# Kernel optimization log

Hardware: AMD Instinct MI355X
Metric: run time of the kernel (lower is better)

The kernel has to match this reference:

```python
import jax, jax.numpy as jnp
import numpy as np

HEADS = 16
LN_EPS = 1e-5


def setup_inputs() -> dict:
    key = jax.random.key(0)
    ks = jax.random.split(key, 4)
    B, S, C, U = 2, 2048, 1024, 1024
    scale = 1.0 / np.sqrt(C)
    return {
        "inputs": jax.random.normal(ks[0], (B, S, C), dtype=jnp.float32),
        "Wq": jax.random.normal(ks[1], (C, U), dtype=jnp.float32) * scale,
        "bq": jnp.zeros((U,), dtype=jnp.float32),
        "Wk": jax.random.normal(ks[2], (C, U), dtype=jnp.float32) * scale,
        "bk": jnp.zeros((U,), dtype=jnp.float32),
        "Wv": jax.random.normal(ks[3], (C, U), dtype=jnp.float32) * scale,
        "bv": jnp.zeros((U,), dtype=jnp.float32),
        "ln_gamma": jnp.ones((S, U), dtype=jnp.float32),
        "ln_beta": jnp.zeros((S, U), dtype=jnp.float32),
    }


def reference(inputs, Wq, bq, Wk, bk, Wv, bv, ln_gamma, ln_beta):
    B, S, C = inputs.shape
    U = Wq.shape[1]
    H = HEADS
    dh = U // H

    Q = inputs @ Wq + bq  # [B,S,U]
    K = inputs @ Wk + bk
    V = inputs @ Wv + bv

    # torch: concat(split(X, U//H, dim=-1), dim=0) -> head-major stacking on batch
    def split_heads(X):
        return jnp.moveaxis(X.reshape(B, S, H, dh), 2, 0).reshape(H * B, S, dh)

    Q_, K_, V_ = split_heads(Q), split_heads(K), split_heads(V)

    scores = jnp.einsum('bqd,bkd->bqk', Q_, K_) / jnp.sqrt(jnp.float32(dh))
    tri = jnp.tril(jnp.ones((S, S), dtype=bool))  # causal mask
    scores = jnp.where(tri[None, :, :], scores, jnp.float32(-1e9))
    attn = jax.nn.softmax(scores, axis=-1)
    out_ = jnp.einsum('bqk,bkd->bqd', attn, V_)  # [H*B,S,dh]

    # inverse: split on batch into H chunks of size B, concat on feature dim
    out = jnp.moveaxis(out_.reshape(H, B, S, dh), 0, 2).reshape(B, S, U)

    out = out + inputs  # residual

    # LayerNorm over normalized_shape=[S, U] (joint seq+feature stats)
    mu = jnp.mean(out, axis=(-2, -1), keepdims=True)
    var = jnp.mean(jnp.square(out - mu), axis=(-2, -1), keepdims=True)
    out = (out - mu) / jnp.sqrt(var + LN_EPS) * ln_gamma + ln_beta
    return out
```

## Files before the change

kernel.cpp:

```cpp
#include <hip/hip_runtime.h>
#include <hip/hip_bf16.h>


typedef __bf16 bf16_t;
typedef __bf16 bf16x8 __attribute__((ext_vector_type(8)));
typedef __bf16 bf16x4 __attribute__((ext_vector_type(4)));
typedef _Float16 f16_t;
typedef _Float16 f16x2 __attribute__((ext_vector_type(2)));
typedef _Float16 f16x4 __attribute__((ext_vector_type(4)));
typedef _Float16 f16x8 __attribute__((ext_vector_type(8)));
typedef float f32x4 __attribute__((ext_vector_type(4)));

constexpr int Bsz = 2;
constexpr int Seq = 2048;
constexpr int Cdim = 1024;
constexpr int Udim = 1024;
constexpr int Hn = 16;
constexpr int Dh = 64;
constexpr int Mrows = Bsz * Seq;
constexpr int PerBatch = Seq * Udim;
constexpr float SCLQ = 0.125f * 1.44269504088896340736f;

__device__ __forceinline__ void gload16(const void* g, void* l)
{
    __builtin_amdgcn_global_load_lds(
        (const __attribute__((address_space(1))) void*)g,
        (__attribute__((address_space(3))) void*)l, 16, 0, 0);
}

__device__ __forceinline__ f16x2 pkrtz(float a, float b)
{
    return __builtin_bit_cast(f16x2, __builtin_amdgcn_cvt_pkrtz(a, b));
}

__global__ __launch_bounds__(256)
void prep(const float* __restrict__ X,
          const float* __restrict__ Wq, const float* __restrict__ Wk,
          const float* __restrict__ Wv,
          bf16_t* __restrict__ Xb,
          bf16_t* __restrict__ Tq, bf16_t* __restrict__ Tk,
          bf16_t* __restrict__ Tv, float* __restrict__ stats)
{
    int z = blockIdx.z;
    int tid = threadIdx.x;
    if (z < 3) {
        const float* W = (z == 0) ? Wq : (z == 1) ? Wk : Wv;
        bf16_t* T = (z == 0) ? Tq : (z == 1) ? Tk : Tv;
        __shared__ bf16_t t[64][65];
        int x0 = blockIdx.x * 64, y0 = blockIdx.y * 64;
        int tx = tid & 63, ty = tid >> 6;
        for (int i = ty; i < 64; i += 4)
            t[i][tx] = (bf16_t)W[(size_t)(y0 + i) * Cdim + x0 + tx];
        __syncthreads();
        for (int i = ty; i < 64; i += 4)
            T[(size_t)(x0 + i) * Cdim + y0 + tx] = t[tx][i];
    } else {
        int bi = blockIdx.y * 16 + blockIdx.x;
        if (bi == 0 && tid < 4) stats[tid] = 0.0f;
        const float4* Xv = (const float4*)X;
#pragma unroll
        for (int k = 0; k < 16; k++) {
            int i = bi * 4096 + k * 256 + tid;
            float4 v = Xv[i];
            bf16x4 o = { (bf16_t)v.x, (bf16_t)v.y, (bf16_t)v.z, (bf16_t)v.w };
            *(bf16x4*)(Xb + (size_t)i * 4) = o;
        }
    }
}

__global__ __launch_bounds__(256)
void gemm_qkv(const bf16_t* __restrict__ X,
              const bf16_t* __restrict__ Wt0, const bf16_t* __restrict__ Wt1,
              const bf16_t* __restrict__ Wt2,
              const float* __restrict__ b0, const float* __restrict__ b1,
              const float* __restrict__ b2,
              f16_t* __restrict__ O0, f16_t* __restrict__ O1, f16_t* __restrict__ O2v)
{
    int z = blockIdx.z;
    const bf16_t* Wt = (z == 0) ? Wt0 : (z == 1) ? Wt1 : Wt2;
    const float* bias = (z == 0) ? b0 : (z == 1) ? b1 : b2;
    float scl = (z == 0) ? SCLQ : 1.0f;

    constexpr int Kd = 1024, Nd = 1024;
    __shared__ __align__(16) bf16_t As[128 * 32];
    __shared__ __align__(16) bf16_t Bs[128 * 32];

    int tid = threadIdx.x;
    int wave = tid >> 6, lane = tid & 63, quad = lane >> 4, l16 = lane & 15;
    int wm = (wave & 1) * 64, wn = (wave >> 1) * 64;
    int m0 = blockIdx.y * 128, n0 = blockIdx.x * 128;

    f32x4 acc[4][4] = {};

    int e0 = wave * 512 + lane * 8;
    int r0 = e0 >> 5, c0 = e0 & 31;
    int e1 = e0 + 2048;
    int r1 = e1 >> 5, c1 = e1 & 31;
    const bf16_t* Ag = X + (size_t)m0 * Kd;
    const bf16_t* Bg = Wt + (size_t)n0 * Kd;
    bf16_t* AsW0 = As + wave * 512;
    bf16_t* AsW1 = As + 2048 + wave * 512;
    bf16_t* BsW0 = Bs + wave * 512;
    bf16_t* BsW1 = Bs + 2048 + wave * 512;

    for (int k0 = 0; k0 < Kd; k0 += 32) {
        gload16(Ag + (size_t)r0 * Kd + k0 + c0, AsW0);
        gload16(Ag + (size_t)r1 * Kd + k0 + c1, AsW1);
        gload16(Bg + (size_t)r0 * Kd + k0 + c0, BsW0);
        gload16(Bg + (size_t)r1 * Kd + k0 + c1, BsW1);
        __syncthreads();

        bf16x8 af[4], bfr[4];
#pragma unroll
        for (int i = 0; i < 4; i++)
            af[i] = *(const bf16x8*)&As[(wm + i * 16 + l16) * 32 + quad * 8];
#pragma unroll
        for (int i = 0; i < 4; i++)
            bfr[i] = *(const bf16x8*)&Bs[(wn + i * 16 + l16) * 32 + quad * 8];
#pragma unroll
        for (int mt = 0; mt < 4; mt++)
#pragma unroll
            for (int nt = 0; nt < 4; nt++)
                acc[mt][nt] = __builtin_amdgcn_mfma_f32_16x16x32_bf16(
                    af[mt], bfr[nt], acc[mt][nt], 0, 0, 0);
        __syncthreads();
    }

    if (z < 2) {
        f16_t* Og = (z == 0) ? O0 : O1;
#pragma unroll
        for (int nt = 0; nt < 4; nt++) {
            int col = n0 + wn + nt * 16 + l16;
            float bv = bias[col];
#pragma unroll
            for (int mt = 0; mt < 4; mt++) {
                int row = m0 + wm + mt * 16 + quad * 4;
#pragma unroll
                for (int r = 0; r < 4; r++)
                    Og[(size_t)(row + r) * Nd + col] = (f16_t)((acc[mt][nt][r] + bv) * scl);
            }
        }
    } else {
        int bb = m0 >> 11;
#pragma unroll
        for (int nt = 0; nt < 4; nt++) {
            int col = n0 + wn + nt * 16 + l16;
            float bv = bias[col];
            int h = col >> 6, d = col & 63;
            f16_t* vbase = O2v + (((size_t)(bb * Hn + h) * Dh + d) << 11);
#pragma unroll
            for (int mt = 0; mt < 4; mt++) {
                int row = m0 + wm + mt * 16 + quad * 4;
                int s = row & (Seq - 1);
                f16x4 pk;
#pragma unroll
                for (int r = 0; r < 4; r++) pk[r] = (f16_t)(acc[mt][nt][r] + bv);
                *(f16x4*)(vbase + s) = pk;
            }
        }
    }
}

__global__ __launch_bounds__(256)
void attn7(const f16_t* __restrict__ Q, const f16_t* __restrict__ K,
           const f16_t* __restrict__ Vt, const float* __restrict__ X,
           bf16_t* __restrict__ R, float* __restrict__ stats)
{
    int id = blockIdx.x;
    int c = id & 7;
    int r8 = id >> 3;
    int g = r8 & 3;
    int kk = r8 >> 2;
    int bh = (g << 3) | c;
    int b = bh >> 4, h = bh & 15;
    int qtile = 31 - kk;

    int tid = threadIdx.x;
    int w = tid >> 6, lane = tid & 63, quad = lane >> 4, l16 = lane & 15;
    size_t bS = (size_t)b * Seq;

    __shared__ f16_t Ks[2][64][72];
    __shared__ f16_t Vs[2][64][72];

    const f16_t* Kg = K + bS * Udim + h * Dh;
    const f16_t* Vg = Vt + ((size_t)(b * Hn + h)) * Dh * Seq;

    int sr = tid >> 2, sc = (tid & 3) * 16;
    int q0 = qtile * 64 + w * 16;
    int qidx = q0 + l16;

    const f16_t* Qp = Q + (bS + qidx) * Udim + h * Dh;
    f16x8 qf[2];
#pragma unroll
    for (int s = 0; s < 2; s++) qf[s] = *(const f16x8*)(Qp + s * 32 + quad * 8);

    f32x4 Oacc[4] = {};
    float lsum = 0.0f;

    const f16_t* kp = Kg + (size_t)sr * Udim + sc;
    const f16_t* vp = Vg + (size_t)sr * Seq + sc;

    {
        f16x8 k0 = *(const f16x8*)kp;
        f16x8 k1 = *(const f16x8*)(kp + 8);
        f16x8 v0 = *(const f16x8*)vp;
        f16x8 v1 = *(const f16x8*)(vp + 8);
        *(f16x8*)&Ks[0][sr][sc] = k0;
        *(f16x8*)&Ks[0][sr][sc + 8] = k1;
        *(f16x8*)&Vs[0][sr][sc] = v0;
        *(f16x8*)&Vs[0][sr][sc + 8] = v1;
        kp += (size_t)64 * Udim;
        vp += 64;
    }
    __syncthreads();

    int buf = 0;
    for (int i = 0; i < qtile; i++) {
        f16x8 nk0 = *(const f16x8*)kp;
        f16x8 nk1 = *(const f16x8*)(kp + 8);
        f16x8 nv0 = *(const f16x8*)vp;
        f16x8 nv1 = *(const f16x8*)(vp + 8);
        kp += (size_t)64 * Udim;
        vp += 64;

        f32x4 st[4];
#pragma unroll
        for (int t = 0; t < 4; t++) {
            f32x4 a = {};
#pragma unroll
            for (int s = 0; s < 2; s++) {
                f16x8 kf = *(const f16x8*)&Ks[buf][t * 16 + l16][s * 32 + quad * 8];
                a = __builtin_amdgcn_mfma_f32_16x16x32_f16(kf, qf[s], a, 0, 0, 0);
            }
            st[t] = a;
        }

        f16x4 pf[4];
#pragma unroll
        for (int t = 0; t < 4; t++) {
            float p0 = exp2f(st[t][0]);
            float p1 = exp2f(st[t][1]);
            float p2 = exp2f(st[t][2]);
            float p3 = exp2f(st[t][3]);
            lsum += (p0 + p1) + (p2 + p3);
            f16x2 lo = pkrtz(p0, p1);
            f16x2 hi = pkrtz(p2, p3);
            pf[t][0] = lo[0]; pf[t][1] = lo[1];
            pf[t][2] = hi[0]; pf[t][3] = hi[1];
        }

#pragma unroll
        for (int t = 0; t < 4; t++)
#pragma unroll
            for (int dt = 0; dt < 4; dt++) {
                f16x4 vf = *(const f16x4*)&Vs[buf][dt * 16 + l16][t * 16 + quad * 4];
                Oacc[dt] = __builtin_amdgcn_mfma_f32_16x16x16f16(vf, pf[t], Oacc[dt], 0, 0, 0);
            }

        *(f16x8*)&Ks[buf ^ 1][sr][sc] = nk0;
        *(f16x8*)&Ks[buf ^ 1][sr][sc + 8] = nk1;
        *(f16x8*)&Vs[buf ^ 1][sr][sc] = nv0;
        *(f16x8*)&Vs[buf ^ 1][sr][sc + 8] = nv1;
        __syncthreads();
        buf ^= 1;
    }

    {
        int kv0 = qtile * 64;
#pragma unroll
        for (int t = 0; t < 4; t++) {
            if (t <= w) {
                f32x4 a = {};
#pragma unroll
                for (int s = 0; s < 2; s++) {
                    f16x8 kf = *(const f16x8*)&Ks[buf][t * 16 + l16][s * 32 + quad * 8];
                    a = __builtin_amdgcn_mfma_f32_16x16x32_f16(kf, qf[s], a, 0, 0, 0);
                }
                f16x4 pfd;
#pragma unroll
                for (int r = 0; r < 4; r++) {
                    float sv = a[r];
                    if (kv0 + t * 16 + quad * 4 + r > qidx) sv = -1e30f;
                    float pv = exp2f(sv);
                    lsum += pv;
                    pfd[r] = (f16_t)pv;
                }
#pragma unroll
                for (int dt = 0; dt < 4; dt++) {
                    f16x4 vf = *(const f16x4*)&Vs[buf][dt * 16 + l16][t * 16 + quad * 4];
                    Oacc[dt] = __builtin_amdgcn_mfma_f32_16x16x16f16(vf, pfd, Oacc[dt], 0, 0, 0);
                }
            }
        }
    }

    lsum += __shfl_xor(lsum, 16);
    lsum += __shfl_xor(lsum, 32);
    float invl = 1.0f / lsum;

    float s_acc = 0.0f, ss_acc = 0.0f;
    const float* Xp = X + (bS + qidx) * Udim + h * Dh;
    bf16_t* Rp = R + (bS + qidx) * Udim + h * Dh;
#pragma unroll
    for (int dt = 0; dt < 4; dt++) {
        f32x4 xv = *(const f32x4*)(Xp + dt * 16 + quad * 4);
        f32x4 o = Oacc[dt] * invl + xv;
        bf16x4 ob;
#pragma unroll
        for (int r = 0; r < 4; r++) {
            ob[r] = (bf16_t)o[r];
            s_acc += o[r];
            ss_acc += o[r] * o[r];
        }
        *(bf16x4*)(Rp + dt * 16 + quad * 4) = ob;
    }

#pragma unroll
    for (int o = 1; o < 64; o <<= 1) {
        s_acc += __shfl_xor(s_acc, o);
        ss_acc += __shfl_xor(ss_acc, o);
    }
    __shared__ float red[8];
    if (lane == 0) { red[w] = s_acc; red[4 + w] = ss_acc; }
    __syncthreads();
    if (tid == 0) {
        atomicAdd(&stats[b], red[0] + red[1] + red[2] + red[3]);
        atomicAdd(&stats[2 + b], red[4] + red[5] + red[6] + red[7]);
    }
}

__global__ __launch_bounds__(256)
void ln_norm(const bf16_t* __restrict__ R, const float* __restrict__ gamma,
             const float* __restrict__ beta, const float* __restrict__ stats,
             float* __restrict__ out)
{
    constexpr float invN = 1.0f / (float)PerBatch;
    float mu[2], inv[2];
#pragma unroll
    for (int b = 0; b < 2; b++) {
        float m = stats[b] * invN;
        float var = stats[2 + b] * invN - m * m;
        mu[b] = m;
        inv[b] = rsqrtf(var + 1e-5f);
    }
    int i = blockIdx.x * 256 + threadIdx.x;
    int f = i * 8;
    int b = f >> 21;
    int su = f & (PerBatch - 1);
    bf16x8 rv = *(const bf16x8*)(R + f);
    float4 g0 = *(const float4*)(gamma + su);
    float4 g1 = *(const float4*)(gamma + su + 4);
    float4 be0 = *(const float4*)(beta + su);
    float4 be1 = *(const float4*)(beta + su + 4);
    float4 o0, o1;
    o0.x = ((float)rv[0] - mu[b]) * inv[b] * g0.x + be0.x;
    o0.y = ((float)rv[1] - mu[b]) * inv[b] * g0.y + be0.y;
    o0.z = ((float)rv[2] - mu[b]) * inv[b] * g0.z + be0.z;
    o0.w = ((float)rv[3] - mu[b]) * inv[b] * g0.w + be0.w;
    o1.x = ((float)rv[4] - mu[b]) * inv[b] * g1.x + be1.x;
    o1.y = ((float)rv[5] - mu[b]) * inv[b] * g1.y + be1.y;
    o1.z = ((float)rv[6] - mu[b]) * inv[b] * g1.z + be1.z;
    o1.w = ((float)rv[7] - mu[b]) * inv[b] * g1.w + be1.w;
    *(float4*)(out + f) = o0;
    *(float4*)(out + f + 4) = o1;
}

extern "C" void kernel_launch(void* const* d_in, const int* in_sizes, int n_in,
                              void* d_out, int out_size, void* d_ws, size_t ws_size,
                              hipStream_t stream)
{
    const float* X     = (const float*)d_in[0];
    const float* Wq    = (const float*)d_in[1];
    const float* bq    = (const float*)d_in[2];
    const float* Wk    = (const float*)d_in[3];
    const float* bk    = (const float*)d_in[4];
    const float* Wv    = (const float*)d_in[5];
    const float* bv    = (const float*)d_in[6];
    const float* gamma = (const float*)d_in[7];
    const float* beta  = (const float*)d_in[8];
    float* out = (float*)d_out;

    char* ws = (char*)d_ws;
    size_t off = 0;
    auto alloc = [&](size_t bytes) -> void* {
        void* p = ws + off;
        off += (bytes + 255) & ~(size_t)255;
        return p;
    };
    bf16_t* Xb = (bf16_t*)alloc((size_t)Mrows * Cdim * 2);
    bf16_t* Tq = (bf16_t*)alloc((size_t)Cdim * Udim * 2);
    bf16_t* Tk = (bf16_t*)alloc((size_t)Cdim * Udim * 2);
    bf16_t* Tv = (bf16_t*)alloc((size_t)Cdim * Udim * 2);
    f16_t*  Qb = (f16_t*)alloc((size_t)Mrows * Udim * 2);
    f16_t*  Kb = (f16_t*)alloc((size_t)Mrows * Udim * 2);
    f16_t*  Vtb = (f16_t*)alloc((size_t)Mrows * Udim * 2);
    bf16_t* Rb = (bf16_t*)alloc((size_t)Mrows * Udim * 2);
    float*  stats = (float*)alloc(4 * sizeof(float));

    prep<<<dim3(16, 16, 4), 256, 0, stream>>>(X, Wq, Wk, Wv, Xb, Tq, Tk, Tv, stats);
    gemm_qkv<<<dim3(8, 32, 3), 256, 0, stream>>>(Xb, Tq, Tk, Tv, bq, bk, bv, Qb, Kb, Vtb);
    attn7<<<dim3(1024), 256, 0, stream>>>(Qb, Kb, Vtb, X, Rb, stats);
    ln_norm<<<dim3(2048), 256, 0, stream>>>(Rb, gamma, beta, stats, out);
}
```

Before: 191.5 us.

## Pair causal q-tiles per block with split-KV groups and async LDS staging

Rewrites the attention kernel so each 512-thread block handles two query tiles (qa and its complement qb), which balances causal work across blocks. Two 256-thread groups split the KV range of the long tile and merge partial outputs and sums through LDS. K/V tiles are now staged with global_load_lds into XOR-swizzled LDS buffers instead of register round-trips, and exp2 uses the hardware builtin. The block uses about 64KB of LDS and a larger thread count, which trades occupancy and extra merge synchronisation for even load and fewer launched blocks.

```diff
diff --git a/kernel.cpp b/kernel.cpp
--- a/kernel.cpp
+++ b/kernel.cpp
@@ -20,6 +20,14 @@
 constexpr int Mrows = Bsz * Seq;
 constexpr int PerBatch = Seq * Udim;
 constexpr float SCLQ = 0.125f * 1.44269504088896340736f;
+
+#if __has_builtin(__builtin_amdgcn_exp2f)
+#define EXP2F(x) __builtin_amdgcn_exp2f(x)
+#else
+#define EXP2F(x) exp2f(x)
+#endif
+
+#define AINL __attribute__((always_inline))
 
 __device__ __forceinline__ void gload16(const void* g, void* l)
 {
@@ -161,158 +169,217 @@
     }
 }
 
-__global__ __launch_bounds__(256)
-void attn7(const f16_t* __restrict__ Q, const f16_t* __restrict__ K,
-           const f16_t* __restrict__ Vt, const float* __restrict__ X,
-           bf16_t* __restrict__ R, float* __restrict__ stats)
+__global__ __launch_bounds__(512, 4)
+void attn12(const f16_t* __restrict__ Q, const f16_t* __restrict__ K,
+            const f16_t* __restrict__ Vt, const float* __restrict__ X,
+            bf16_t* __restrict__ R, float* __restrict__ stats)
 {
     int id = blockIdx.x;
     int c = id & 7;
-    int r8 = id >> 3;
-    int g = r8 & 3;
-    int kk = r8 >> 2;
+    int rr = id >> 3;
+    int g = rr & 3;
+    int pi = rr >> 2;
     int bh = (g << 3) | c;
     int b = bh >> 4, h = bh & 15;
-    int qtile = 31 - kk;
+    int qa = 31 - pi, qb = pi, split = 15 - pi;
 
     int tid = threadIdx.x;
-    int w = tid >> 6, lane = tid & 63, quad = lane >> 4, l16 = lane & 15;
+    int grp = tid >> 8;
+    int w = (tid >> 6) & 3;
+    int lane = tid & 63, quad = lane >> 4, l16 = lane & 15;
     size_t bS = (size_t)b * Seq;
 
-    __shared__ f16_t Ks[2][64][72];
-    __shared__ f16_t Vs[2][64][72];
+    __shared__ __align__(16) char ldsRaw[65600];
+    f16_t* KsBase = (f16_t*)(ldsRaw + grp * 32768);
+    f16_t* VsBase = (f16_t*)(ldsRaw + grp * 32768 + 16384);
+    float* cmbO   = (float*)(ldsRaw + 32768);
+    float* cmbLS  = (float*)(ldsRaw + 49152);
+    float* red    = (float*)(ldsRaw + 65536);
 
     const f16_t* Kg = K + bS * Udim + h * Dh;
     const f16_t* Vg = Vt + ((size_t)(b * Hn + h)) * Dh * Seq;
 
-    int sr = tid >> 2, sc = (tid & 3) * 16;
-    int q0 = qtile * 64 + w * 16;
-    int qidx = q0 + l16;
-
-    const f16_t* Qp = Q + (bS + qidx) * Udim + h * Dh;
-    f16x8 qf[2];
-#pragma unroll
-    for (int s = 0; s < 2; s++) qf[s] = *(const f16x8*)(Qp + s * 32 + quad * 8);
-
-    f32x4 Oacc[4] = {};
-    float lsum = 0.0f;
-
-    const f16_t* kp = Kg + (size_t)sr * Udim + sc;
-    const f16_t* vp = Vg + (size_t)sr * Seq + sc;
-
-    {
-        f16x8 k0 = *(const f16x8*)kp;
-        f16x8 k1 = *(const f16x8*)(kp + 8);
-        f16x8 v0 = *(const f16x8*)vp;
-        f16x8 v1 = *(const f16x8*)(vp + 8);
-        *(f16x8*)&Ks[0][sr][sc] = k0;
-        *(f16x8*)&Ks[0][sr][sc + 8] = k1;
-        *(f16x8*)&Vs[0][sr][sc] = v0;
-        *(f16x8*)&Vs[0][sr][sc + 8] = v1;
-        kp += (size_t)64 * Udim;
-        vp += 64;
-    }
-    __syncthreads();
-
-    int buf = 0;
-    for (int i = 0; i < qtile; i++) {
-        f16x8 nk0 = *(const f16x8*)kp;
-        f16x8 nk1 = *(const f16x8*)(kp + 8);
-        f16x8 nv0 = *(const f16x8*)vp;
-        f16x8 nv1 = *(const f16x8*)(vp + 8);
-        kp += (size_t)64 * Udim;
-        vp += 64;
-
+    int srow = w * 8 + (lane >> 3);
+    int schunk = (lane & 7) ^ ((lane >> 3) & 7);
+
+    int qidxA = qa * 64 + w * 16 + l16;
+    int qidxB = qb * 64 + w * 16 + l16;
+    const f16_t* QpA = Q + (bS + qidxA) * Udim + h * Dh;
+    const f16_t* QpB = Q + (bS + qidxB) * Udim + h * Dh;
+    f16x8 qfA[2], qfB[2];
+#pragma unroll
+    for (int s2 = 0; s2 < 2; s2++) {
+        qfA[s2] = *(const f16x8*)(QpA + s2 * 32 + quad * 8);
+        qfB[s2] = *(const f16x8*)(QpB + s2 * 32 + quad * 8);
+    }
+
+    int m = l16 & 7;
+    int kO0 = l16 * 64 + ((quad ^ m) << 3);
+    int kO1 = l16 * 64 + (((4 + quad) ^ m) << 3);
+    int vO[4];
+#pragma unroll
+    for (int t = 0; t < 4; t++)
+        vO[t] = l16 * 64 + (((t * 32 + quad * 8) ^ (m << 4)) >> 1);
+
+    f32x4 OA[4] = {}, OB[4] = {};
+    float lsA = 0.0f, lsB = 0.0f;
+
+    auto STAGE = [&](int nb, int tl) AINL {
+        const f16_t* kp = Kg + (size_t)(tl * 64 + srow) * Udim + schunk * 8;
+        const f16_t* vp = Vg + (size_t)srow * Seq + tl * 64 + schunk * 8;
+        f16_t* kd = KsBase + nb * 4096;
+        f16_t* vd = VsBase + nb * 4096;
+        gload16(kp, kd + w * 512);
+        gload16(kp + (size_t)32 * Udim, kd + 2048 + w * 512);
+        gload16(vp, vd + w * 512);
+        gload16(vp + (size_t)32 * Seq, vd + 2048 + w * 512);
+    };
+
+    auto CN = [&](int buf, const f16x8 (&qf)[2], f32x4 (&O)[4], float& ls) AINL {
+        const f16_t* Kb = KsBase + buf * 4096;
+        const f16_t* Vb = VsBase + buf * 4096;
         f32x4 st[4];
 #pragma unroll
         for (int t = 0; t < 4; t++) {
+            f16x8 kf0 = *(const f16x8*)&Kb[kO0 + t * 1024];
+            f16x8 kf1 = *(const f16x8*)&Kb[kO1 + t * 1024];
             f32x4 a = {};
-#pragma unroll
-            for (int s = 0; s < 2; s++) {
-                f16x8 kf = *(const f16x8*)&Ks[buf][t * 16 + l16][s * 32 + quad * 8];
-                a = __builtin_amdgcn_mfma_f32_16x16x32_f16(kf, qf[s], a, 0, 0, 0);
-            }
+            a = __builtin_amdgcn_mfma_f32_16x16x32_f16(kf0, qf[0], a, 0, 0, 0);
+            a = __builtin_amdgcn_mfma_f32_16x16x32_f16(kf1, qf[1], a, 0, 0, 0);
             st[t] = a;
         }
-
         f16x4 pf[4];
 #pragma unroll
         for (int t = 0; t < 4; t++) {
-            float p0 = exp2f(st[t][0]);
-            float p1 = exp2f(st[t][1]);
-            float p2 = exp2f(st[t][2]);
-            float p3 = exp2f(st[t][3]);
-            lsum += (p0 + p1) + (p2 + p3);
+            float p0 = EXP2F(st[t][0]);
+            float p1 = EXP2F(st[t][1]);
+            float p2 = EXP2F(st[t][2]);
+            float p3 = EXP2F(st[t][3]);
+            ls += (p0 + p1) + (p2 + p3);
             f16x2 lo = pkrtz(p0, p1);
             f16x2 hi = pkrtz(p2, p3);
             pf[t][0] = lo[0]; pf[t][1] = lo[1];
             pf[t][2] = hi[0]; pf[t][3] = hi[1];
         }
-
 #pragma unroll
         for (int t = 0; t < 4; t++)
 #pragma unroll
             for (int dt = 0; dt < 4; dt++) {
-                f16x4 vf = *(const f16x4*)&Vs[buf][dt * 16 + l16][t * 16 + quad * 4];
-                Oacc[dt] = __builtin_amdgcn_mfma_f32_16x16x16f16(vf, pf[t], Oacc[dt], 0, 0, 0);
-            }
-
-        *(f16x8*)&Ks[buf ^ 1][sr][sc] = nk0;
-        *(f16x8*)&Ks[buf ^ 1][sr][sc + 8] = nk1;
-        *(f16x8*)&Vs[buf ^ 1][sr][sc] = nv0;
-        *(f16x8*)&Vs[buf ^ 1][sr][sc + 8] = nv1;
-        __syncthreads();
-        buf ^= 1;
-    }
-
-    {
-        int kv0 = qtile * 64;
+                f16x4 vf = *(const f16x4*)&Vb[vO[t] + dt * 1024];
+                O[dt] = __builtin_amdgcn_mfma_f32_16x16x16f16(vf, pf[t], O[dt], 0, 0, 0);
+            }
+    };
+
+    auto CM = [&](int buf, const f16x8 (&qf)[2], f32x4 (&O)[4], float& ls,
+                  int kv0, int qidx) AINL {
+        const f16_t* Kb = KsBase + buf * 4096;
+        const f16_t* Vb = VsBase + buf * 4096;
 #pragma unroll
         for (int t = 0; t < 4; t++) {
             if (t <= w) {
+                f16x8 kf0 = *(const f16x8*)&Kb[kO0 + t * 1024];
+                f16x8 kf1 = *(const f16x8*)&Kb[kO1 + t * 1024];
                 f32x4 a = {};
-#pragma unroll
-                for (int s = 0; s < 2; s++) {
-                    f16x8 kf = *(const f16x8*)&Ks[buf][t * 16 + l16][s * 32 + quad * 8];
-                    a = __builtin_amdgcn_mfma_f32_16x16x32_f16(kf, qf[s], a, 0, 0, 0);
+                a = __builtin_amdgcn_mfma_f32_16x16x32_f16(kf0, qf[0], a, 0, 0, 0);
+                a = __builtin_amdgcn_mfma_f32_16x16x32_f16(kf1, qf[1], a, 0, 0, 0);
+                f16x4 pfd;
+#pragma unroll
+                for (int r2 = 0; r2 < 4; r2++) {
+                    float sv = a[r2];
+                    if (kv0 + t * 16 + quad * 4 + r2 > qidx) sv = -1e30f;
+                    float pv = EXP2F(sv);
+                    ls += pv;
+                    pfd[r2] = (f16_t)pv;
                 }
-                f16x4 pfd;
-#pragma unroll
-                for (int r = 0; r < 4; r++) {
-                    float sv = a[r];
-                    if (kv0 + t * 16 + quad * 4 + r > qidx) sv = -1e30f;
-                    float pv = exp2f(sv);
-                    lsum += pv;
-                    pfd[r] = (f16_t)pv;
+#pragma unroll
+                for (int dt = 0; dt < 4; dt++) {
+                    f16x4 vf = *(const f16x4*)&Vb[vO[t] + dt * 1024];
+                    O[dt] = __builtin_amdgcn_mfma_f32_16x16x16f16(vf, pfd, O[dt], 0, 0, 0);
                 }
-#pragma unroll
-                for (int dt = 0; dt < 4; dt++) {
-                    f16x4 vf = *(const f16x4*)&Vs[buf][dt * 16 + l16][t * 16 + quad * 4];
-                    Oacc[dt] = __builtin_amdgcn_mfma_f32_16x16x16f16(vf, pfd, Oacc[dt], 0, 0, 0);
-                }
-            }
-        }
-    }
-
-    lsum += __shfl_xor(lsum, 16);
-    lsum += __shfl_xor(lsum, 32);
-    float invl = 1.0f / lsum;
+            }
+        }
+    };
+
+    STAGE(0, (grp == 0) ? 0 : split);
+    __syncthreads();
+
+    int r = 0;
+    auto ROUND = [&](int buf) AINL {
+        if (r < 16) {
+            int rn = r + 1;
+            int tl = (grp == 0) ? ((rn <= qb) ? rn : rn - qb - 1) : (split + rn);
+            STAGE(buf ^ 1, tl);
+        }
+        if (grp == 0) {
+            if (r < qb)       CN(buf, qfB, OB, lsB);
+            else if (r == qb) CM(buf, qfB, OB, lsB, qb * 64, qidxB);
+            else if (r < 16)  CN(buf, qfA, OA, lsA);
+        } else {
+            if (r < 16)       CN(buf, qfA, OA, lsA);
+            else              CM(buf, qfA, OA, lsA, qa * 64, qidxA);
+        }
+        __syncthreads();
+        r++;
+    };
+
+    for (int i = 0; i < 8; i++) { ROUND(0); ROUND(1); }
+    ROUND(0);
+
+    lsA += __shfl_xor(lsA, 16);
+    lsA += __shfl_xor(lsA, 32);
 
     float s_acc = 0.0f, ss_acc = 0.0f;
-    const float* Xp = X + (bS + qidx) * Udim + h * Dh;
-    bf16_t* Rp = R + (bS + qidx) * Udim + h * Dh;
-#pragma unroll
-    for (int dt = 0; dt < 4; dt++) {
-        f32x4 xv = *(const f32x4*)(Xp + dt * 16 + quad * 4);
-        f32x4 o = Oacc[dt] * invl + xv;
-        bf16x4 ob;
-#pragma unroll
-        for (int r = 0; r < 4; r++) {
-            ob[r] = (bf16_t)o[r];
-            s_acc += o[r];
-            ss_acc += o[r] * o[r];
-        }
-        *(bf16x4*)(Rp + dt * 16 + quad * 4) = ob;
+
+    if (grp == 1) {
+        float* po = cmbO + w * 1024 + lane * 16;
+#pragma unroll
+        for (int dt = 0; dt < 4; dt++)
+            *(f32x4*)(po + dt * 4) = OA[dt];
+        if (lane < 16) cmbLS[w * 16 + l16] = lsA;
+    } else {
+        lsB += __shfl_xor(lsB, 16);
+        lsB += __shfl_xor(lsB, 32);
+        float invB = 1.0f / lsB;
+        const float* XpB = X + (bS + qidxB) * Udim + h * Dh;
+        bf16_t* RpB = R + (bS + qidxB) * Udim + h * Dh;
+#pragma unroll
+        for (int dt = 0; dt < 4; dt++) {
+            f32x4 xv = *(const f32x4*)(XpB + dt * 16 + quad * 4);
+            f32x4 o = OB[dt] * invB + xv;
+            bf16x4 ob;
+#pragma unroll
+            for (int r2 = 0; r2 < 4; r2++) {
+                ob[r2] = (bf16_t)o[r2];
+                s_acc += o[r2];
+                ss_acc += o[r2] * o[r2];
+            }
+            *(bf16x4*)(RpB + dt * 16 + quad * 4) = ob;
+        }
+    }
+    __syncthreads();
+
+    if (grp == 0) {
+        const float* po = cmbO + w * 1024 + lane * 16;
+#pragma unroll
+        for (int dt = 0; dt < 4; dt++)
+            OA[dt] += *(const f32x4*)(po + dt * 4);
+        lsA += cmbLS[w * 16 + l16];
+        float invA = 1.0f / lsA;
+        const float* XpA = X + (bS + qidxA) * Udim + h * Dh;
+        bf16_t* RpA = R + (bS + qidxA) * Udim + h * Dh;
+#pragma unroll
+        for (int dt = 0; dt < 4; dt++) {
+            f32x4 xv = *(const f32x4*)(XpA + dt * 16 + quad * 4);
+            f32x4 o = OA[dt] * invA + xv;
+            bf16x4 ob;
+#pragma unroll
+            for (int r2 = 0; r2 < 4; r2++) {
+                ob[r2] = (bf16_t)o[r2];
+                s_acc += o[r2];
+                ss_acc += o[r2] * o[r2];
+            }
+            *(bf16x4*)(RpA + dt * 16 + quad * 4) = ob;
+        }
     }
 
 #pragma unroll
@@ -320,12 +387,15 @@
         s_acc += __shfl_xor(s_acc, o);
         ss_acc += __shfl_xor(ss_acc, o);
     }
-    __shared__ float red[8];
-    if (lane == 0) { red[w] = s_acc; red[4 + w] = ss_acc; }
+    int w8 = tid >> 6;
+    if (lane == 0) { red[w8] = s_acc; red[8 + w8] = ss_acc; }
     __syncthreads();
     if (tid == 0) {
-        atomicAdd(&stats[b], red[0] + red[1] + red[2] + red[3]);
-        atomicAdd(&stats[2 + b], red[4] + red[5] + red[6] + red[7]);
+        float s = 0.0f, ss = 0.0f;
+#pragma unroll
+        for (int i = 0; i < 8; i++) { s += red[i]; ss += red[8 + i]; }
+        atomicAdd(&stats[b], s);
+        atomicAdd(&stats[2 + b], ss);
     }
 }
 
@@ -399,6 +469,6 @@
 
     prep<<<dim3(16, 16, 4), 256, 0, stream>>>(X, Wq, Wk, Wv, Xb, Tq, Tk, Tv, stats);
     gemm_qkv<<<dim3(8, 32, 3), 256, 0, stream>>>(Xb, Tq, Tk, Tv, bq, bk, bv, Qb, Kb, Vtb);
-    attn7<<<dim3(1024), 256, 0, stream>>>(Qb, Kb, Vtb, X, Rb, stats);
+    attn12<<<dim3(512), 512, 0, stream>>>(Qb, Kb, Vtb, X, Rb, stats);
     ln_norm<<<dim3(2048), 256, 0, stream>>>(Rb, gamma, beta, stats, out);
 }
```

After: 185.1 us. 3.4% less time.
